# Performance work log

Hardware: AMD Instinct MI355X
Metric: run time of the kernel (lower is better)

## Reference

```python
import jax, jax.numpy as jnp
import numpy as np

N_NEURONS = 2048
IN_DIM = 1024
OUT_DIM = 1024
TOKENS = 4096
TIME_STEPS = 3
DENSITY = 0.25


def setup_inputs() -> dict:
    key = jax.random.key(0)
    ks = jax.random.split(key, 10)
    x = jax.random.normal(ks[0], (TOKENS, IN_DIM), dtype=jnp.float32)
    W_in = jax.random.normal(ks[1], (N_NEURONS, IN_DIM), dtype=jnp.float32) * (1.0 / np.sqrt(IN_DIM))
    b_in = jax.random.normal(ks[2], (N_NEURONS,), dtype=jnp.float32) * 0.01
    weights = jax.random.normal(ks[3], (N_NEURONS, N_NEURONS), dtype=jnp.float32) * 0.3
    J = jax.random.normal(ks[4], (N_NEURONS, N_NEURONS), dtype=jnp.float32) * 0.1
    theta = jax.random.uniform(ks[5], (N_NEURONS,), dtype=jnp.float32) * 1.0 + 0.25
    lam = jnp.asarray(0.35, dtype=jnp.float32)
    # connection mask: rand < density, zero diagonal (buffer, fixed)
    m = (jax.random.uniform(ks[6], (N_NEURONS, N_NEURONS)) < DENSITY).astype(jnp.float32)
    mask = m * (1.0 - jnp.eye(N_NEURONS, dtype=jnp.float32))
    noise_raw = jax.random.normal(ks[7], (TIME_STEPS, TOKENS, N_NEURONS), dtype=jnp.float32)
    W_out = jax.random.normal(ks[8], (OUT_DIM, N_NEURONS), dtype=jnp.float32) * (1.0 / np.sqrt(N_NEURONS))
    b_out = jax.random.normal(ks[9], (OUT_DIM,), dtype=jnp.float32) * 0.01
    return {"x": x, "W_in": W_in, "b_in": b_in, "weights": weights, "J": J,
            "theta": theta, "lam": lam, "mask": mask, "noise_raw": noise_raw,
            "W_out": W_out, "b_out": b_out, "time_steps": TIME_STEPS}


def reference(x, W_in, b_in, weights, J, theta, lam, mask, noise_raw, W_out, b_out, time_steps):
    # input projection: [tokens, in_dim] -> [tokens, n]
    state = x @ W_in.T + b_in
    eff_w = weights * mask          # [n, n]
    J_m = J * mask                  # [n, n]
    T = jnp.abs(jnp.sin(2.0 * theta))  # temperature [n]
    for t in range(time_steps):
        signal = state @ eff_w                     # [tokens, n]
        s = jnp.tanh(state)
        # einsum('bi,ij,bj->bj', s, J_m, s) == (s @ J_m) * s
        delta = (s @ J_m) * s                      # [tokens, n]
        noise = noise_raw[t] * T * 0.1             # [tokens, n]
        state = jnp.tanh(signal + lam * delta + noise)
    return state @ W_out.T + b_out
```

## Files before the change

kernel.cpp:

```cpp
#include <hip/hip_runtime.h>
#include <hip/hip_fp16.h>

#define TOKENS 4096
#define NN 2048
#define IN_DIM 1024
#define OUT_DIM 1024
#define TSTEPS 3

typedef _Float16 half8 __attribute__((ext_vector_type(8)));
typedef _Float16 half4 __attribute__((ext_vector_type(4)));
typedef float f32x4 __attribute__((ext_vector_type(4)));

__device__ __forceinline__ void gload_lds16(const void* g, void* l) {
    __builtin_amdgcn_global_load_lds(
        (const __attribute__((address_space(1))) unsigned*)g,
        (__attribute__((address_space(3))) unsigned*)l, 16, 0, 0);
}

__global__ __launch_bounds__(512, 2)
void dual_gemm(const _Float16* __restrict__ A0, const _Float16* __restrict__ B0,
               float* __restrict__ C0,
               const _Float16* __restrict__ A1, const _Float16* __restrict__ B1,
               float* __restrict__ C1)
{
    __shared__ __align__(16) _Float16 lds[4 * 16384];
    const int tid  = threadIdx.x;
    const int wid  = tid >> 6;
    const int lane = tid & 63;

    int bid = blockIdx.x;
    const int g = bid >> 7;
    bid &= 127;
    const int bx = bid & 7;
    const int by = bid >> 3;
    const _Float16* __restrict__ A = g ? A1 : A0;
    const _Float16* __restrict__ B = g ? B1 : B0;
    float* __restrict__ C = g ? C1 : C0;
    const int brow = by << 8;
    const int bcol = bx << 8;

    const int sr = tid >> 2;
    const int sc = ((tid & 3) ^ ((tid >> 3) & 3)) << 3;
    const _Float16* gA = A + (size_t)(brow + sr) * NN + sc;
    const _Float16* gB = B + (size_t)(bcol + sr) * NN + sc;
    const int ldst = wid << 9;

    auto stageA = [&](int u) {
        _Float16* l = lds + (u & 3) * 16384;
        const _Float16* a = gA + u * 32;
        gload_lds16(a,            l + ldst);
        gload_lds16(a + 128 * NN, l + 4096 + ldst);
    };
    auto stageB = [&](int u) {
        _Float16* l = lds + (u & 3) * 16384;
        const _Float16* b = gB + u * 32;
        gload_lds16(b,            l + 8192  + ldst);
        gload_lds16(b + 128 * NN, l + 12288 + ldst);
    };

    const int wr = (wid >> 2) << 7;
    const int wc = (wid & 3) << 6;
    const int lr = lane & 15;
    const int swz = ((lane >> 4) ^ ((lr >> 1) & 3)) << 3;
    const int aRd = (wr + lr) * 32 + swz;
    const int bRd = 8192 + (wc + lr) * 32 + swz;

    f32x4 acc[8][4];
#pragma unroll
    for (int m = 0; m < 8; ++m)
#pragma unroll
        for (int n = 0; n < 4; ++n) acc[m][n] = (f32x4){0.f, 0.f, 0.f, 0.f};

    stageA(0); stageB(0); stageA(1); stageB(1); stageA(2); stageB(2);
    asm volatile("s_waitcnt vmcnt(8)" ::: "memory");
    __builtin_amdgcn_s_barrier();

    for (int t = 0; t < 64; ++t) {
        const _Float16* lb = lds + (t & 3) * 16384;

        half8 af[4], bf[4];
#pragma unroll
        for (int m = 0; m < 4; ++m)
            af[m] = *(const half8*)&lb[aRd + (m << 9)];
#pragma unroll
        for (int n = 0; n < 4; ++n)
            bf[n] = *(const half8*)&lb[bRd + (n << 9)];
        if (t < 61) stageA(t + 3);
        __builtin_amdgcn_s_barrier();
        asm volatile("s_waitcnt lgkmcnt(0)" ::: "memory");
        __builtin_amdgcn_sched_barrier(0);
        __builtin_amdgcn_s_setprio(1);
#pragma unroll
        for (int m = 0; m < 4; ++m)
#pragma unroll
            for (int n = 0; n < 4; ++n)
                acc[m][n] = __builtin_amdgcn_mfma_f32_16x16x32_f16(af[m], bf[n], acc[m][n], 0, 0, 0);
        __builtin_amdgcn_s_setprio(0);
        __builtin_amdgcn_sched_barrier(0);
        __builtin_amdgcn_s_barrier();

#pragma unroll
        for (int m = 0; m < 4; ++m)
            af[m] = *(const half8*)&lb[aRd + ((m + 4) << 9)];
        if (t < 61) stageB(t + 3);
        __builtin_amdgcn_s_barrier();
        asm volatile("s_waitcnt lgkmcnt(0)" ::: "memory");
        __builtin_amdgcn_sched_barrier(0);
        __builtin_amdgcn_s_setprio(1);
#pragma unroll
        for (int m = 0; m < 4; ++m)
#pragma unroll
            for (int n = 0; n < 4; ++n)
                acc[m + 4][n] = __builtin_amdgcn_mfma_f32_16x16x32_f16(af[m], bf[n], acc[m + 4][n], 0, 0, 0);
        __builtin_amdgcn_s_setprio(0);
        __builtin_amdgcn_sched_barrier(0);

        if (t < 61)      asm volatile("s_waitcnt vmcnt(8)" ::: "memory");
        else if (t == 61) asm volatile("s_waitcnt vmcnt(4)" ::: "memory");
        else if (t == 62) asm volatile("s_waitcnt vmcnt(0)" ::: "memory");
        __builtin_amdgcn_s_barrier();
    }

    const int cr = (lane >> 4) << 2;
    const int cc = lane & 15;
#pragma unroll
    for (int m = 0; m < 8; ++m) {
#pragma unroll
        for (int n = 0; n < 4; ++n) {
            const size_t o0 = (size_t)(brow + wr + m * 16 + cr) * NN
                            + (bcol + wc + n * 16 + cc);
#pragma unroll
            for (int j = 0; j < 4; ++j)
                C[o0 + (size_t)j * NN] = acc[m][n][j];
        }
    }
}

template<int EPI>
__global__ __launch_bounds__(256)
void gemm_bt(const _Float16* __restrict__ A, const _Float16* __restrict__ B,
             float* __restrict__ C, const float* __restrict__ bias,
             _Float16* __restrict__ oSta, _Float16* __restrict__ oS,
             int M, int N, int K)
{
    __shared__ _Float16 As[128 * 32];
    __shared__ _Float16 Bs[128 * 32];
    const int tid  = threadIdx.x;
    const int wid  = tid >> 6;
    const int lane = tid & 63;
    const int wr = (wid >> 1) * 64;
    const int wc = (wid & 1) * 64;
    const int brow = blockIdx.y * 128;
    const int bcol = blockIdx.x * 128;

    f32x4 acc[4][4];
#pragma unroll
    for (int m = 0; m < 4; ++m)
#pragma unroll
        for (int n = 0; n < 4; ++n) acc[m][n] = (f32x4){0.f, 0.f, 0.f, 0.f};

    const int ldr = tid >> 2;
    const int ldc = (tid & 3) * 8;
    const int wbase = (wid << 4) * 32;
    const int kq = (lane >> 4) * 8;
    const int lr = lane & 15;

    for (int k0 = 0; k0 < K; k0 += 32) {
        __syncthreads();
        gload_lds16(A + (size_t)(brow + ldr) * K + k0 + ldc, As + wbase);
        gload_lds16(A + (size_t)(brow + 64 + ldr) * K + k0 + ldc, As + 64 * 32 + wbase);
        gload_lds16(B + (size_t)(bcol + ldr) * K + k0 + ldc, Bs + wbase);
        gload_lds16(B + (size_t)(bcol + 64 + ldr) * K + k0 + ldc, Bs + 64 * 32 + wbase);
        __syncthreads();

        half8 af[4], bf[4];
#pragma unroll
        for (int m = 0; m < 4; ++m)
            af[m] = *(const half8*)&As[(wr + m * 16 + lr) * 32 + kq];
#pragma unroll
        for (int n = 0; n < 4; ++n)
            bf[n] = *(const half8*)&Bs[(wc + n * 16 + lr) * 32 + kq];
#pragma unroll
        for (int m = 0; m < 4; ++m)
#pragma unroll
            for (int n = 0; n < 4; ++n)
                acc[m][n] = __builtin_amdgcn_mfma_f32_16x16x32_f16(af[m], bf[n], acc[m][n], 0, 0, 0);
    }

    const int cr = (lane >> 4) * 4;
    const int cc = lane & 15;
#pragma unroll
    for (int m = 0; m < 4; ++m) {
#pragma unroll
        for (int n = 0; n < 4; ++n) {
            const int ccol = bcol + wc + n * 16 + cc;
#pragma unroll
            for (int j = 0; j < 4; ++j) {
                const int crow = brow + wr + m * 16 + cr + j;
                float v = acc[m][n][j];
                const size_t o = (size_t)crow * N + ccol;
                if (EPI == 1) {
                    v += bias[ccol];
                    oSta[o] = (_Float16)v;
                    oS[o] = (_Float16)tanhf(v);
                } else {
                    C[o] = v + bias[ccol];
                }
            }
        }
    }
}

__global__ void cvt_f16(const float* __restrict__ in, _Float16* __restrict__ out, int n4) {
    int i = blockIdx.x * blockDim.x + threadIdx.x;
    if (i < n4) {
        f32x4 v = *(const f32x4*)&in[(size_t)i * 4];
        half4 h;
        h[0] = (_Float16)v[0]; h[1] = (_Float16)v[1];
        h[2] = (_Float16)v[2]; h[3] = (_Float16)v[3];
        *(half4*)&out[(size_t)i * 4] = h;
    }
}

__global__ void transmul2(const float* __restrict__ W, const float* __restrict__ J,
                          const float* __restrict__ Mk,
                          _Float16* __restrict__ effT, _Float16* __restrict__ JmT) {
    __shared__ float tw[32][33];
    __shared__ float tj[32][33];
    const int bx = blockIdx.x * 32, by = blockIdx.y * 32;
    const int tx = threadIdx.x, ty0 = threadIdx.y;
#pragma unroll
    for (int r = 0; r < 4; ++r) {
        int ty = ty0 + r * 8;
        size_t idx = (size_t)(by + ty) * NN + bx + tx;
        float mv = Mk[idx];
        tw[ty][tx] = W[idx] * mv;
        tj[ty][tx] = J[idx] * mv;
    }
    __syncthreads();
#pragma unroll
    for (int r = 0; r < 4; ++r) {
        int ty = ty0 + r * 8;
        size_t o = (size_t)(bx + ty) * NN + by + tx;
        effT[o] = (_Float16)tw[tx][ty];
        JmT[o]  = (_Float16)tj[tx][ty];
    }
}

__global__ void tsc_kernel(const float* __restrict__ theta, float* __restrict__ Tsc) {
    int i = blockIdx.x * blockDim.x + threadIdx.x;
    if (i < NN) Tsc[i] = fabsf(sinf(2.0f * theta[i])) * 0.1f;
}

__global__ void step_kernel(const float* __restrict__ signal, const float* __restrict__ sJ,
                            const float* __restrict__ noise, const float* __restrict__ Tsc,
                            const float* __restrict__ lamp,
                            _Float16* __restrict__ stateH, _Float16* __restrict__ sH) {
    const int i4 = blockIdx.x * blockDim.x + threadIdx.x;
    const float lam = lamp[0];
    const size_t base = (size_t)i4 * 4;
    f32x4 sg = *(const f32x4*)&signal[base];
    f32x4 dj = *(const f32x4*)&sJ[base];
    f32x4 nz = *(const f32x4*)&noise[base];
    const int col4 = (int)(base & (NN - 1));
    f32x4 tv = *(const f32x4*)&Tsc[col4];
    half4 so = *(const half4*)&sH[base];
    half4 hs, hn;
#pragma unroll
    for (int j = 0; j < 4; ++j) {
        float s = (float)so[j];
        float arg = sg[j] + lam * (dj[j] * s) + nz[j] * tv[j];
        float st = tanhf(arg);
        hs[j] = (_Float16)st;
        hn[j] = (_Float16)tanhf(st);
    }
    *(half4*)&stateH[base] = hs;
    *(half4*)&sH[base] = hn;
}

extern "C" void kernel_launch(void* const* d_in, const int* in_sizes, int n_in,
                              void* d_out, int out_size, void* d_ws, size_t ws_size,
                              hipStream_t stream) {
    const float* x       = (const float*)d_in[0];
    const float* W_in    = (const float*)d_in[1];
    const float* b_in    = (const float*)d_in[2];
    const float* weights = (const float*)d_in[3];
    const float* Jmat    = (const float*)d_in[4];
    const float* theta   = (const float*)d_in[5];
    const float* lam     = (const float*)d_in[6];
    const float* mask    = (const float*)d_in[7];
    const float* noise   = (const float*)d_in[8];
    const float* W_out   = (const float*)d_in[9];
    const float* b_out   = (const float*)d_in[10];
    float* out = (float*)d_out;

    char* w = (char*)d_ws;
    auto alloc = [&](size_t b) { char* p = w; w += (b + 255) & ~(size_t)255; return p; };
    _Float16* xh     = (_Float16*)alloc((size_t)TOKENS * IN_DIM * 2);
    _Float16* WinH   = (_Float16*)alloc((size_t)NN * IN_DIM * 2);
    _Float16* WoutH  = (_Float16*)alloc((size_t)OUT_DIM * NN * 2);
    _Float16* effT   = (_Float16*)alloc((size_t)NN * NN * 2);
    _Float16* JmT    = (_Float16*)alloc((size_t)NN * NN * 2);
    _Float16* stateH = (_Float16*)alloc((size_t)TOKENS * NN * 2);
    _Float16* sH     = (_Float16*)alloc((size_t)TOKENS * NN * 2);
    float* Tsc       = (float*)alloc((size_t)NN * 4);
    float* signal    = (float*)alloc((size_t)TOKENS * NN * 4);
    float* sJ        = (float*)alloc((size_t)TOKENS * NN * 4);

    cvt_f16<<<TOKENS * IN_DIM / 4 / 256, 256, 0, stream>>>(x, xh, TOKENS * IN_DIM / 4);
    cvt_f16<<<NN * IN_DIM / 4 / 256, 256, 0, stream>>>(W_in, WinH, NN * IN_DIM / 4);
    cvt_f16<<<OUT_DIM * NN / 4 / 256, 256, 0, stream>>>(W_out, WoutH, OUT_DIM * NN / 4);
    transmul2<<<dim3(NN / 32, NN / 32), dim3(32, 8), 0, stream>>>(weights, Jmat, mask, effT, JmT);
    tsc_kernel<<<NN / 256, 256, 0, stream>>>(theta, Tsc);

    gemm_bt<1><<<dim3(NN / 128, TOKENS / 128), 256, 0, stream>>>(
        xh, WinH, nullptr, b_in, stateH, sH, TOKENS, NN, IN_DIM);

    for (int t = 0; t < TSTEPS; ++t) {
        dual_gemm<<<256, 512, 0, stream>>>(stateH, effT, signal, sH, JmT, sJ);
        step_kernel<<<TOKENS * NN / 4 / 256, 256, 0, stream>>>(
            signal, sJ, noise + (size_t)t * TOKENS * NN, Tsc, lam, stateH, sH);
    }

    gemm_bt<2><<<dim3(OUT_DIM / 128, TOKENS / 128), 256, 0, stream>>>(
        stateH, WoutH, out, b_out, nullptr, nullptr, TOKENS, OUT_DIM, NN);
}
```

Baseline: 391.8 us.

## Shrink dual GEMM tile to 128x256 with 256 threads and triple buffering

Changes the dual GEMM block tile from 256x256 with 8 waves to 128x256 with 4 waves. It doubles the grid to 512 blocks, which gives better occupancy and CU coverage on a 256-CU part. The LDS pipeline goes from 4 stages (prefetch depth 3) to 3 stages (prefetch depth 2), cutting shared memory per block. A blockIdx remap interleaves blocks, probably to improve L2 locality across the two GEMMs. The cost is more global traffic per FLOP and less latency hiding from the shallower prefetch.

```diff
diff --git a/kernel.cpp b/kernel.cpp
--- a/kernel.cpp
+++ b/kernel.cpp
@@ -17,26 +17,27 @@
         (__attribute__((address_space(3))) unsigned*)l, 16, 0, 0);
 }
 
-__global__ __launch_bounds__(512, 2)
+__global__ __launch_bounds__(256, 2)
 void dual_gemm(const _Float16* __restrict__ A0, const _Float16* __restrict__ B0,
                float* __restrict__ C0,
                const _Float16* __restrict__ A1, const _Float16* __restrict__ B1,
                float* __restrict__ C1)
 {
-    __shared__ __align__(16) _Float16 lds[4 * 16384];
+    __shared__ __align__(16) _Float16 lds[3 * 12288];
     const int tid  = threadIdx.x;
     const int wid  = tid >> 6;
     const int lane = tid & 63;
 
-    int bid = blockIdx.x;
-    const int g = bid >> 7;
-    bid &= 127;
+    const int raw  = blockIdx.x;
+    const int widx = (raw & 7) * 64 + (raw >> 3);
+    const int g    = widx >> 8;
+    const int bid  = widx & 255;
+    const int by = bid >> 3;
     const int bx = bid & 7;
-    const int by = bid >> 3;
     const _Float16* __restrict__ A = g ? A1 : A0;
     const _Float16* __restrict__ B = g ? B1 : B0;
     float* __restrict__ C = g ? C1 : C0;
-    const int brow = by << 8;
+    const int brow = by << 7;
     const int bcol = bx << 8;
 
     const int sr = tid >> 2;
@@ -45,25 +46,26 @@
     const _Float16* gB = B + (size_t)(bcol + sr) * NN + sc;
     const int ldst = wid << 9;
 
-    auto stageA = [&](int u) {
-        _Float16* l = lds + (u & 3) * 16384;
+    auto stageA = [&](int u, int b) {
+        _Float16* l = lds + b * 12288;
         const _Float16* a = gA + u * 32;
-        gload_lds16(a,            l + ldst);
-        gload_lds16(a + 128 * NN, l + 4096 + ldst);
+        gload_lds16(a,           l + ldst);
+        gload_lds16(a + 64 * NN, l + 2048 + ldst);
     };
-    auto stageB = [&](int u) {
-        _Float16* l = lds + (u & 3) * 16384;
-        const _Float16* b = gB + u * 32;
-        gload_lds16(b,            l + 8192  + ldst);
-        gload_lds16(b + 128 * NN, l + 12288 + ldst);
+    auto stageB = [&](int u, int b) {
+        _Float16* l = lds + b * 12288 + 4096;
+        const _Float16* p = gB + u * 32;
+        gload_lds16(p,            l + ldst);
+        gload_lds16(p + 64 * NN,  l + 2048 + ldst);
+        gload_lds16(p + 128 * NN, l + 4096 + ldst);
+        gload_lds16(p + 192 * NN, l + 6144 + ldst);
     };
 
-    const int wr = (wid >> 2) << 7;
-    const int wc = (wid & 3) << 6;
+    const int wc = wid << 6;
     const int lr = lane & 15;
     const int swz = ((lane >> 4) ^ ((lr >> 1) & 3)) << 3;
-    const int aRd = (wr + lr) * 32 + swz;
-    const int bRd = 8192 + (wc + lr) * 32 + swz;
+    const int aRd = lr * 32 + swz;
+    const int bRd = 4096 + (wc + lr) * 32 + swz;
 
     f32x4 acc[8][4];
 #pragma unroll
@@ -71,12 +73,15 @@
 #pragma unroll
         for (int n = 0; n < 4; ++n) acc[m][n] = (f32x4){0.f, 0.f, 0.f, 0.f};
 
-    stageA(0); stageB(0); stageA(1); stageB(1); stageA(2); stageB(2);
-    asm volatile("s_waitcnt vmcnt(8)" ::: "memory");
+    stageA(0, 0); stageB(0, 0);
+    stageA(1, 1); stageB(1, 1);
+    asm volatile("s_waitcnt vmcnt(6)" ::: "memory");
     __builtin_amdgcn_s_barrier();
 
+    int cur = 0;
     for (int t = 0; t < 64; ++t) {
-        const _Float16* lb = lds + (t & 3) * 16384;
+        const _Float16* lb = lds + cur * 12288;
+        const int nb = (cur == 0) ? 2 : cur - 1;
 
         half8 af[4], bf[4];
 #pragma unroll
@@ -85,7 +90,7 @@
 #pragma unroll
         for (int n = 0; n < 4; ++n)
             bf[n] = *(const half8*)&lb[bRd + (n << 9)];
-        if (t < 61) stageA(t + 3);
+        if (t < 62) stageA(t + 2, nb);
         __builtin_amdgcn_s_barrier();
         asm volatile("s_waitcnt lgkmcnt(0)" ::: "memory");
         __builtin_amdgcn_sched_barrier(0);
@@ -102,7 +107,7 @@
 #pragma unroll
         for (int m = 0; m < 4; ++m)
             af[m] = *(const half8*)&lb[aRd + ((m + 4) << 9)];
-        if (t < 61) stageB(t + 3);
+        if (t < 62) stageB(t + 2, nb);
         __builtin_amdgcn_s_barrier();
         asm volatile("s_waitcnt lgkmcnt(0)" ::: "memory");
         __builtin_amdgcn_sched_barrier(0);
@@ -115,10 +120,10 @@
         __builtin_amdgcn_s_setprio(0);
         __builtin_amdgcn_sched_barrier(0);
 
-        if (t < 61)      asm volatile("s_waitcnt vmcnt(8)" ::: "memory");
-        else if (t == 61) asm volatile("s_waitcnt vmcnt(4)" ::: "memory");
+        if (t < 62)       asm volatile("s_waitcnt vmcnt(6)" ::: "memory");
         else if (t == 62) asm volatile("s_waitcnt vmcnt(0)" ::: "memory");
         __builtin_amdgcn_s_barrier();
+        cur = (cur == 2) ? 0 : cur + 1;
     }
 
     const int cr = (lane >> 4) << 2;
@@ -127,7 +132,7 @@
     for (int m = 0; m < 8; ++m) {
 #pragma unroll
         for (int n = 0; n < 4; ++n) {
-            const size_t o0 = (size_t)(brow + wr + m * 16 + cr) * NN
+            const size_t o0 = (size_t)(brow + m * 16 + cr) * NN
                             + (bcol + wc + n * 16 + cc);
 #pragma unroll
             for (int j = 0; j < 4; ++j)
@@ -317,7 +322,7 @@
         xh, WinH, nullptr, b_in, stateH, sH, TOKENS, NN, IN_DIM);
 
     for (int t = 0; t < TSTEPS; ++t) {
-        dual_gemm<<<256, 512, 0, stream>>>(stateH, effT, signal, sH, JmT, sJ);
+        dual_gemm<<<512, 256, 0, stream>>>(stateH, effT, signal, sH, JmT, sJ);
         step_kernel<<<TOKENS * NN / 4 / 256, 256, 0, stream>>>(
             signal, sJ, noise + (size_t)t * TOKENS * NN, Tsc, lam, stateH, sH);
     }
```

Measured after the change: 386.3 us. Within noise of the previous version (-1.4%).

## Restructure dual GEMM to K=64 double-buffered tiles with four-phase MFMA schedule

Applied to the files above, without the earlier changes.

Switches the dual GEMM mainloop from a 4-stage ring of K=32 tiles to a 2-stage double buffer of K=64 tiles. Each iteration is split into four quadrant phases that interleave LDS fragment reads, global-to-LDS prefetch and MFMA bursts. It also remaps block IDs so consecutive workgroups are spread across the grid, and adopts an 8-way XOR swizzle matching the wider rows. The intent is fewer barriers per unit of K and better overlap of loads with MFMA, at the cost of a shallower prefetch depth and more registers held for fragments.

```diff
diff --git a/kernel.cpp b/kernel.cpp
--- a/kernel.cpp
+++ b/kernel.cpp
@@ -18,52 +18,56 @@
 }
 
 __global__ __launch_bounds__(512, 2)
-void dual_gemm(const _Float16* __restrict__ A0, const _Float16* __restrict__ B0,
+void dual_gemm(const _Float16* __restrict__ A0g, const _Float16* __restrict__ B0g,
                float* __restrict__ C0,
-               const _Float16* __restrict__ A1, const _Float16* __restrict__ B1,
+               const _Float16* __restrict__ A1g, const _Float16* __restrict__ B1g,
                float* __restrict__ C1)
 {
-    __shared__ __align__(16) _Float16 lds[4 * 16384];
+    __shared__ __align__(16) _Float16 lds[2 * 32768];
     const int tid  = threadIdx.x;
     const int wid  = tid >> 6;
     const int lane = tid & 63;
 
-    int bid = blockIdx.x;
-    const int g = bid >> 7;
-    bid &= 127;
+    const int raw  = blockIdx.x;
+    const int widx = (raw & 7) * 32 + (raw >> 3);
+    const int g    = widx >> 7;
+    const int bid  = widx & 127;
+    const int by = bid >> 3;
     const int bx = bid & 7;
-    const int by = bid >> 3;
-    const _Float16* __restrict__ A = g ? A1 : A0;
-    const _Float16* __restrict__ B = g ? B1 : B0;
+    const _Float16* __restrict__ A = g ? A1g : A0g;
+    const _Float16* __restrict__ B = g ? B1g : B0g;
     float* __restrict__ C = g ? C1 : C0;
     const int brow = by << 8;
     const int bcol = bx << 8;
 
-    const int sr = tid >> 2;
-    const int sc = ((tid & 3) ^ ((tid >> 3) & 3)) << 3;
+    const int sr = tid >> 3;
+    const int sc = ((tid & 7) ^ (sr & 7)) << 3;
     const _Float16* gA = A + (size_t)(brow + sr) * NN + sc;
     const _Float16* gB = B + (size_t)(bcol + sr) * NN + sc;
     const int ldst = wid << 9;
 
-    auto stageA = [&](int u) {
-        _Float16* l = lds + (u & 3) * 16384;
-        const _Float16* a = gA + u * 32;
-        gload_lds16(a,            l + ldst);
-        gload_lds16(a + 128 * NN, l + 4096 + ldst);
+    auto stA = [&](int T, int h) {
+        _Float16* l = lds + (T & 1) * 32768 + h * 8192;
+        const _Float16* p = gA + (size_t)(h << 7) * NN + (T << 6);
+        gload_lds16(p,           l + ldst);
+        gload_lds16(p + 64 * NN, l + 4096 + ldst);
     };
-    auto stageB = [&](int u) {
-        _Float16* l = lds + (u & 3) * 16384;
-        const _Float16* b = gB + u * 32;
-        gload_lds16(b,            l + 8192  + ldst);
-        gload_lds16(b + 128 * NN, l + 12288 + ldst);
+    auto stB = [&](int T, int h) {
+        _Float16* l = lds + (T & 1) * 32768 + 16384 + h * 8192;
+        const _Float16* p = gB + (size_t)(h << 7) * NN + (T << 6);
+        gload_lds16(p,           l + ldst);
+        gload_lds16(p + 64 * NN, l + 4096 + ldst);
     };
 
     const int wr = (wid >> 2) << 7;
     const int wc = (wid & 3) << 6;
     const int lr = lane & 15;
-    const int swz = ((lane >> 4) ^ ((lr >> 1) & 3)) << 3;
-    const int aRd = (wr + lr) * 32 + swz;
-    const int bRd = 8192 + (wc + lr) * 32 + swz;
+    const int lq = lane >> 4;
+    const int x7 = lr & 7;
+    const int c0 = (lq ^ x7) << 3;
+    const int c1 = ((4 + lq) ^ x7) << 3;
+    const int aRow = (wr + lr) << 6;
+    const int bRow = 16384 + ((wc + lr) << 6);
 
     f32x4 acc[8][4];
 #pragma unroll
@@ -71,57 +75,104 @@
 #pragma unroll
         for (int n = 0; n < 4; ++n) acc[m][n] = (f32x4){0.f, 0.f, 0.f, 0.f};
 
-    stageA(0); stageB(0); stageA(1); stageB(1); stageA(2); stageB(2);
+    half8 af[4][2], b0f[2][2], b1f[2][2];
+
+    stA(0, 0); stA(0, 1); stB(0, 0); stB(0, 1);
+    stA(1, 0); stA(1, 1); stB(1, 0); stB(1, 1);
     asm volatile("s_waitcnt vmcnt(8)" ::: "memory");
     __builtin_amdgcn_s_barrier();
-
-    for (int t = 0; t < 64; ++t) {
-        const _Float16* lb = lds + (t & 3) * 16384;
-
-        half8 af[4], bf[4];
-#pragma unroll
-        for (int m = 0; m < 4; ++m)
-            af[m] = *(const half8*)&lb[aRd + (m << 9)];
-#pragma unroll
-        for (int n = 0; n < 4; ++n)
-            bf[n] = *(const half8*)&lb[bRd + (n << 9)];
-        if (t < 61) stageA(t + 3);
+    asm volatile("" ::: "memory");
+
+    for (int T = 0; T < 32; ++T) {
+        const _Float16* lb = lds + (T & 1) * 32768;
+
+#pragma unroll
+        for (int m = 0; m < 4; ++m) {
+            af[m][0] = *(const half8*)&lb[aRow + (m << 10) + c0];
+            af[m][1] = *(const half8*)&lb[aRow + (m << 10) + c1];
+        }
+#pragma unroll
+        for (int n = 0; n < 2; ++n) {
+            b0f[n][0] = *(const half8*)&lb[bRow + (n << 10) + c0];
+            b0f[n][1] = *(const half8*)&lb[bRow + (n << 10) + c1];
+        }
         __builtin_amdgcn_s_barrier();
         asm volatile("s_waitcnt lgkmcnt(0)" ::: "memory");
         __builtin_amdgcn_sched_barrier(0);
         __builtin_amdgcn_s_setprio(1);
 #pragma unroll
-        for (int m = 0; m < 4; ++m)
-#pragma unroll
-            for (int n = 0; n < 4; ++n)
-                acc[m][n] = __builtin_amdgcn_mfma_f32_16x16x32_f16(af[m], bf[n], acc[m][n], 0, 0, 0);
+        for (int kk = 0; kk < 2; ++kk)
+#pragma unroll
+            for (int m = 0; m < 4; ++m)
+#pragma unroll
+                for (int n = 0; n < 2; ++n)
+                    acc[m][n] = __builtin_amdgcn_mfma_f32_16x16x32_f16(af[m][kk], b0f[n][kk], acc[m][n], 0, 0, 0);
         __builtin_amdgcn_s_setprio(0);
         __builtin_amdgcn_sched_barrier(0);
         __builtin_amdgcn_s_barrier();
-
-#pragma unroll
-        for (int m = 0; m < 4; ++m)
-            af[m] = *(const half8*)&lb[aRd + ((m + 4) << 9)];
-        if (t < 61) stageB(t + 3);
+        asm volatile("" ::: "memory");
+
+#pragma unroll
+        for (int n = 0; n < 2; ++n) {
+            b1f[n][0] = *(const half8*)&lb[bRow + ((n + 2) << 10) + c0];
+            b1f[n][1] = *(const half8*)&lb[bRow + ((n + 2) << 10) + c1];
+        }
         __builtin_amdgcn_s_barrier();
         asm volatile("s_waitcnt lgkmcnt(0)" ::: "memory");
         __builtin_amdgcn_sched_barrier(0);
         __builtin_amdgcn_s_setprio(1);
 #pragma unroll
-        for (int m = 0; m < 4; ++m)
-#pragma unroll
-            for (int n = 0; n < 4; ++n)
-                acc[m + 4][n] = __builtin_amdgcn_mfma_f32_16x16x32_f16(af[m], bf[n], acc[m + 4][n], 0, 0, 0);
+        for (int kk = 0; kk < 2; ++kk)
+#pragma unroll
+            for (int m = 0; m < 4; ++m)
+#pragma unroll
+                for (int n = 0; n < 2; ++n)
+                    acc[m][n + 2] = __builtin_amdgcn_mfma_f32_16x16x32_f16(af[m][kk], b1f[n][kk], acc[m][n + 2], 0, 0, 0);
         __builtin_amdgcn_s_setprio(0);
         __builtin_amdgcn_sched_barrier(0);
-
-        if (t < 61)      asm volatile("s_waitcnt vmcnt(8)" ::: "memory");
-        else if (t == 61) asm volatile("s_waitcnt vmcnt(4)" ::: "memory");
-        else if (t == 62) asm volatile("s_waitcnt vmcnt(0)" ::: "memory");
-        __builtin_amdgcn_s_barrier();
-    }
-
-    const int cr = (lane >> 4) << 2;
+        __builtin_amdgcn_s_barrier();
+        asm volatile("" ::: "memory");
+
+#pragma unroll
+        for (int m = 0; m < 4; ++m) {
+            af[m][0] = *(const half8*)&lb[aRow + ((m + 4) << 10) + c0];
+            af[m][1] = *(const half8*)&lb[aRow + ((m + 4) << 10) + c1];
+        }
+        if (T < 30) { stB(T + 2, 0); stB(T + 2, 1); }
+        __builtin_amdgcn_s_barrier();
+        asm volatile("s_waitcnt lgkmcnt(0)" ::: "memory");
+        __builtin_amdgcn_sched_barrier(0);
+        __builtin_amdgcn_s_setprio(1);
+#pragma unroll
+        for (int kk = 0; kk < 2; ++kk)
+#pragma unroll
+            for (int m = 0; m < 4; ++m)
+#pragma unroll
+                for (int n = 0; n < 2; ++n)
+                    acc[m + 4][n] = __builtin_amdgcn_mfma_f32_16x16x32_f16(af[m][kk], b0f[n][kk], acc[m + 4][n], 0, 0, 0);
+        __builtin_amdgcn_s_setprio(0);
+        __builtin_amdgcn_sched_barrier(0);
+        __builtin_amdgcn_s_barrier();
+        asm volatile("" ::: "memory");
+
+        if (T < 30) { stA(T + 2, 0); stA(T + 2, 1); }
+        __builtin_amdgcn_s_setprio(1);
+#pragma unroll
+        for (int kk = 0; kk < 2; ++kk)
+#pragma unroll
+            for (int m = 0; m < 4; ++m)
+#pragma unroll
+                for (int n = 0; n < 2; ++n)
+                    acc[m + 4][n + 2] = __builtin_amdgcn_mfma_f32_16x16x32_f16(af[m][kk], b1f[n][kk], acc[m + 4][n + 2], 0, 0, 0);
+        __builtin_amdgcn_s_setprio(0);
+        __builtin_amdgcn_sched_barrier(0);
+        if (T < 30)       asm volatile("s_waitcnt vmcnt(8)" ::: "memory");
+        else if (T == 30) asm volatile("s_waitcnt vmcnt(0)" ::: "memory");
+        __builtin_amdgcn_s_barrier();
+        asm volatile("" ::: "memory");
+    }
+
+    const int cr = lq << 2;
     const int cc = lane & 15;
 #pragma unroll
     for (int m = 0; m < 8; ++m) {
```

Result: faster. 381.3 us (-2.7%).
